# Kernel tuning notes

Hardware: AMD Instinct MI355X
Metric: run time of the kernel (lower is better)

Reference implementation:

```python
import jax, jax.numpy as jnp
import numpy as np

B, T, C = 2, 2048, 2048
H, D = 16, 128
ROPE_THETA = 100000.0


def _rms_norm(x):
    eps = jnp.asarray(jnp.finfo(x.dtype).eps, x.dtype)
    var = jnp.mean(jnp.square(x), axis=-1, keepdims=True)
    return x * jax.lax.rsqrt(var + eps)


def _apply_rotary(x, cos, sin):
    # x: [B,T,H,D]; cos/sin: [T,1,D//2] broadcasting over (B, H)
    d = x.shape[-1] // 2
    x1, x2 = x[..., :d], x[..., d:]
    y1 = x1 * cos + x2 * sin
    y2 = -x1 * sin + x2 * cos
    return jnp.concatenate([y1, y2], axis=-1)


def setup_inputs() -> dict:
    key = jax.random.key(0)
    ks = jax.random.split(key, 5)
    x = jax.random.normal(ks[0], (B, T, C), dtype=jnp.float32)
    # rotary table (caller-provided, already offset-applied)
    inv_freq = 1.0 / (ROPE_THETA ** (np.arange(0, D // 2, dtype=np.float32) / (D // 2)))
    t = np.arange(T, dtype=np.float32)
    freqs = np.outer(t, inv_freq)  # [T, D//2]
    cos = jnp.asarray(np.cos(freqs))[:, None, :]  # [T,1,D//2]
    sin = jnp.asarray(np.sin(freqs))[:, None, :]
    std = 0.02
    Wq = jax.random.normal(ks[1], (C, C), dtype=jnp.float32) * std
    Wk = jax.random.normal(ks[2], (C, C), dtype=jnp.float32) * std
    Wv = jax.random.normal(ks[3], (C, C), dtype=jnp.float32) * std
    Wo = jax.random.normal(ks[4], (C, C), dtype=jnp.float32) * std
    return {"x": x, "cos": cos, "sin": sin, "Wq": Wq, "Wk": Wk, "Wv": Wv, "Wo": Wo}


def reference(x, cos, sin, Wq, Wk, Wv, Wo):
    b, t, _ = x.shape
    # torch Linear: y = x @ W.T
    q = (x @ Wq.T).reshape(b, t, H, D)
    k = (x @ Wk.T).reshape(b, t, H, D)
    v = (x @ Wv.T).reshape(b, t, H, D)
    # qk RMSNorm (qk_norm=True)
    q = _rms_norm(q)
    k = _rms_norm(k)
    # rotary
    q = _apply_rotary(q, cos, sin)
    k = _apply_rotary(k, cos, sin)
    # causal SDPA, scale = 1/sqrt(D)
    scale = 1.0 / jnp.sqrt(jnp.asarray(D, x.dtype))
    scores = jnp.einsum('bthd,bshd->bhts', q, k) * scale  # [B,H,T,T]
    causal = jnp.tril(jnp.ones((t, t), dtype=bool))
    scores = jnp.where(causal[None, None], scores, jnp.asarray(-jnp.inf, x.dtype))
    attn = jax.nn.softmax(scores, axis=-1)
    o = jnp.einsum('bhts,bshd->bthd', attn, v).reshape(b, t, H * D)
    return o @ Wo.T
```

## Files before the change

kernel.cpp:

```cpp
#include <hip/hip_runtime.h>

using u16 = unsigned short;
typedef __attribute__((ext_vector_type(8))) short short8;
typedef __attribute__((ext_vector_type(4))) float f32x4;

#define DEV __device__ __forceinline__

DEV float bf2f(u16 u) { union { unsigned i; float f; } v; v.i = (unsigned)u << 16; return v.f; }
DEV u16 f2bf(float f) {
  union { float f; unsigned i; } v; v.f = f;
  return (u16)((v.i + 0x7fffu + ((v.i >> 16) & 1u)) >> 16);
}
DEV void async16(void* lds, const void* g) {
  __builtin_amdgcn_global_load_lds((const __attribute__((address_space(1))) void*)g,
                                   (__attribute__((address_space(3))) void*)lds, 16, 0, 0);
}

__global__ __launch_bounds__(256) void cvt_bf16(const float* __restrict__ in,
                                                u16* __restrict__ out, int n) {
  int i = (blockIdx.x * 256 + threadIdx.x) * 8;
  if (i >= n) return;
  const float4* p = (const float4*)(in + i);
  float4 a = p[0], b = p[1];
  short8 o;
  o[0] = (short)f2bf(a.x); o[1] = (short)f2bf(a.y);
  o[2] = (short)f2bf(a.z); o[3] = (short)f2bf(a.w);
  o[4] = (short)f2bf(b.x); o[5] = (short)f2bf(b.y);
  o[6] = (short)f2bf(b.z); o[7] = (short)f2bf(b.w);
  *(short8*)(out + i) = o;
}

template <bool BF16OUT>
DEV void gemm_body(const u16* __restrict__ A, const u16* __restrict__ Bw,
                   void* __restrict__ C, u16* As, u16* Bs) {
  constexpr int KD = 2048, N = 2048;
  const int tid = threadIdx.x, lane = tid & 63, w = tid >> 6;
  const int wm = (w >> 1) * 64, wn = (w & 1) * 64;
  const int lr = lane & 15, lk = lane >> 4;
  const size_t m0 = (size_t)blockIdx.y * 128, n0 = (size_t)blockIdx.x * 128;

  f32x4 acc[4][4];
#pragma unroll
  for (int i = 0; i < 4; ++i)
#pragma unroll
    for (int j = 0; j < 4; ++j) acc[i][j] = (f32x4){0.f, 0.f, 0.f, 0.f};

  const int bo0 = tid * 16;
  for (int kt = 0; kt < KD; kt += 32) {
#pragma unroll
    for (int i = 0; i < 2; ++i) {
      int bo = i * 4096 + bo0;
      int row = bo >> 6, cb = bo & 63;
      async16((char*)As + i * 4096 + w * 1024,
              (const char*)A + ((m0 + row) * KD + kt) * 2 + cb);
    }
#pragma unroll
    for (int i = 0; i < 2; ++i) {
      int bo = i * 4096 + bo0;
      int row = bo >> 6, cb = bo & 63;
      async16((char*)Bs + i * 4096 + w * 1024,
              (const char*)Bw + ((n0 + row) * KD + kt) * 2 + cb);
    }
    __syncthreads();
    short8 a[4], b[4];
#pragma unroll
    for (int mi = 0; mi < 4; ++mi)
      a[mi] = *(const short8*)(As + (wm + mi * 16 + lr) * 32 + lk * 8);
#pragma unroll
    for (int ni = 0; ni < 4; ++ni)
      b[ni] = *(const short8*)(Bs + (wn + ni * 16 + lr) * 32 + lk * 8);
#pragma unroll
    for (int mi = 0; mi < 4; ++mi)
#pragma unroll
      for (int ni = 0; ni < 4; ++ni)
        acc[mi][ni] =
            __builtin_amdgcn_mfma_f32_16x16x32_bf16(a[mi], b[ni], acc[mi][ni], 0, 0, 0);
    __syncthreads();
  }
#pragma unroll
  for (int mi = 0; mi < 4; ++mi)
#pragma unroll
    for (int ni = 0; ni < 4; ++ni)
#pragma unroll
      for (int r = 0; r < 4; ++r) {
        size_t row = m0 + wm + mi * 16 + lk * 4 + r;
        size_t col = n0 + wn + ni * 16 + lr;
        if constexpr (BF16OUT)
          ((u16*)C)[row * N + col] = f2bf(acc[mi][ni][r]);
        else
          ((float*)C)[row * N + col] = acc[mi][ni][r];
      }
}

__global__ __launch_bounds__(256) void gemm_qkv(
    const u16* __restrict__ X, const u16* __restrict__ Wq, const u16* __restrict__ Wk,
    const u16* __restrict__ Wv, u16* __restrict__ Qo, u16* __restrict__ Ko,
    u16* __restrict__ Vo) {
  __shared__ u16 As[128 * 32], Bs[128 * 32];
  const u16* W = blockIdx.z == 0 ? Wq : (blockIdx.z == 1 ? Wk : Wv);
  u16* C = blockIdx.z == 0 ? Qo : (blockIdx.z == 1 ? Ko : Vo);
  gemm_body<true>(X, W, C, As, Bs);
}

__global__ __launch_bounds__(256) void gemm_out(const u16* __restrict__ A,
                                                const u16* __restrict__ W,
                                                float* __restrict__ C) {
  __shared__ u16 As[128 * 32], Bs[128 * 32];
  gemm_body<false>(A, W, C, As, Bs);
}

__global__ __launch_bounds__(256) void rmsrope(u16* __restrict__ q, u16* __restrict__ k,
                                               const float* __restrict__ cosb,
                                               const float* __restrict__ sinb) {
  int gw = blockIdx.x * 4 + (threadIdx.x >> 6);
  int lane = threadIdx.x & 63;
  u16* base = q;
  float pre = 0.088388347648318447f * 1.4426950408889634f;
  if (gw >= 65536) { base = k; gw -= 65536; pre = 1.0f; }
  int bt = gw >> 4, h = gw & 15, t = bt & 2047;
  u16* p = base + (size_t)bt * 2048 + h * 128;
  float x1 = bf2f(p[lane]), x2 = bf2f(p[lane + 64]);
  float ss = x1 * x1 + x2 * x2;
#pragma unroll
  for (int m = 1; m < 64; m <<= 1) ss += __shfl_xor(ss, m, 64);
  float rn = rsqrtf(ss * (1.0f / 128.0f) + 1.1920929e-7f) * pre;
  float c = cosb[t * 64 + lane], s = sinb[t * 64 + lane];
  float y1 = (x1 * c + x2 * s) * rn;
  float y2 = (x2 * c - x1 * s) * rn;
  p[lane] = f2bf(y1);
  p[lane + 64] = f2bf(y2);
}

__global__ __launch_bounds__(256) void transpose_v(const u16* __restrict__ v,
                                                   u16* __restrict__ vt) {
  __shared__ u16 tile[64][72];
  int bh = blockIdx.z, b = bh >> 4, h = bh & 15;
  int t0 = blockIdx.x * 64, d0 = blockIdx.y * 64;
  int tid = threadIdx.x;
  int rr = tid >> 3, ch = tid & 7;
#pragma unroll
  for (int p = 0; p < 2; ++p) {
    int t = rr + p * 32;
    const u16* src = v + ((size_t)(b * 2048 + t0 + t) * 2048 + h * 128 + d0 + ch * 8);
    *(short8*)&tile[t][ch * 8] = *(const short8*)src;
  }
  __syncthreads();
#pragma unroll
  for (int p = 0; p < 2; ++p) {
    int d = rr + p * 32;
    int oc = ch * 8;
    short8 val;
#pragma unroll
    for (int j = 0; j < 8; ++j) val[j] = (short)tile[oc + j][d];
    *(short8*)(vt + ((size_t)(bh * 128 + d0 + d) * 2048 + t0 + oc)) = val;
  }
}

__global__ __launch_bounds__(256) void attn_fwd(const u16* __restrict__ Q,
                                                const u16* __restrict__ K,
                                                const u16* __restrict__ Vt,
                                                u16* __restrict__ O) {
  __shared__ u16 Ks[64 * 128];
  __shared__ u16 Vs[128 * 64];
  __shared__ u16 Ps[4][16 * 72];
  const int tid = threadIdx.x, lane = tid & 63, w = tid >> 6;
  const int lr = lane & 15, lk = lane >> 4;
  const int bh = blockIdx.y, b = bh >> 4, h = bh & 15;
  const int q0 = blockIdx.x * 64;
  const int qw = q0 + w * 16;

  short8 aq[4];
  const u16* qptr = Q + ((size_t)(b * 2048 + qw + lr)) * 2048 + h * 128;
#pragma unroll
  for (int kk = 0; kk < 4; ++kk) aq[kk] = *(const short8*)(qptr + kk * 32 + lk * 8);

  float mrow[4], lrow[4];
  f32x4 o[8];
#pragma unroll
  for (int r = 0; r < 4; ++r) { mrow[r] = -__builtin_inff(); lrow[r] = 0.f; }
#pragma unroll
  for (int nd = 0; nd < 8; ++nd) o[nd] = (f32x4){0.f, 0.f, 0.f, 0.f};

  const char* kbase = (const char*)(K + ((size_t)b * 2048) * 2048 + h * 128);
  const char* vbase = (const char*)(Vt + (size_t)bh * 128 * 2048);
  const int ntiles = blockIdx.x + 1;
  const int bo0 = tid * 16;

  for (int kt = 0; kt < ntiles; ++kt) {
    const int kv0 = kt * 64;
#pragma unroll
    for (int i = 0; i < 4; ++i) {
      int bo = i * 4096 + bo0;
      int r = bo >> 8, cb = bo & 255;
      async16((char*)Ks + i * 4096 + w * 1024,
              kbase + (size_t)(kv0 + r) * 4096 + (cb ^ ((r & 7) << 4)));
    }
#pragma unroll
    for (int i = 0; i < 4; ++i) {
      int bo = i * 4096 + bo0;
      int d = bo >> 7, cb = bo & 127;
      async16((char*)Vs + i * 4096 + w * 1024,
              vbase + (size_t)d * 4096 + (size_t)kv0 * 2 + (cb ^ ((d & 7) << 4)));
    }
    __syncthreads();

    f32x4 s[4];
#pragma unroll
    for (int n = 0; n < 4; ++n) {
      s[n] = (f32x4){0.f, 0.f, 0.f, 0.f};
#pragma unroll
      for (int kk = 0; kk < 4; ++kk) {
        int row = n * 16 + lr;
        int cb = kk * 64 + lk * 16;
        short8 bk = *(const short8*)((const char*)Ks + row * 256 + (cb ^ ((row & 7) << 4)));
        s[n] = __builtin_amdgcn_mfma_f32_16x16x32_bf16(aq[kk], bk, s[n], 0, 0, 0);
      }
    }
    if (kt == ntiles - 1) {
#pragma unroll
      for (int n = 0; n < 4; ++n)
#pragma unroll
        for (int r = 0; r < 4; ++r) {
          int col = kv0 + n * 16 + lr;
          int row = qw + lk * 4 + r;
          if (col > row) s[n][r] = -__builtin_inff();
        }
    }
    float al[4];
#pragma unroll
    for (int r = 0; r < 4; ++r) {
      float mx = fmaxf(fmaxf(s[0][r], s[1][r]), fmaxf(s[2][r], s[3][r]));
      mx = fmaxf(mx, __shfl_xor(mx, 1, 64));
      mx = fmaxf(mx, __shfl_xor(mx, 2, 64));
      mx = fmaxf(mx, __shfl_xor(mx, 4, 64));
      mx = fmaxf(mx, __shfl_xor(mx, 8, 64));
      float mn = fmaxf(mrow[r], mx);
      al[r] = exp2f(mrow[r] - mn);
      mrow[r] = mn;
    }
    float rs[4] = {0.f, 0.f, 0.f, 0.f};
#pragma unroll
    for (int n = 0; n < 4; ++n)
#pragma unroll
      for (int r = 0; r < 4; ++r) {
        float pv = exp2f(s[n][r] - mrow[r]);
        s[n][r] = pv;
        rs[r] += pv;
      }
#pragma unroll
    for (int r = 0; r < 4; ++r) {
      float t = rs[r];
      t += __shfl_xor(t, 1, 64); t += __shfl_xor(t, 2, 64);
      t += __shfl_xor(t, 4, 64); t += __shfl_xor(t, 8, 64);
      lrow[r] = lrow[r] * al[r] + t;
    }
#pragma unroll
    for (int nd = 0; nd < 8; ++nd)
#pragma unroll
      for (int r = 0; r < 4; ++r) o[nd][r] *= al[r];

    u16* pw = Ps[w];
#pragma unroll
    for (int n = 0; n < 4; ++n)
#pragma unroll
      for (int r = 0; r < 4; ++r)
        pw[(lk * 4 + r) * 72 + n * 16 + lr] = f2bf(s[n][r]);

#pragma unroll
    for (int kk = 0; kk < 2; ++kk) {
      short8 pa = *(const short8*)(pw + lr * 72 + kk * 32 + lk * 8);
#pragma unroll
      for (int nd = 0; nd < 8; ++nd) {
        int dr = nd * 16 + lr;
        int cb = kk * 64 + lk * 16;
        short8 bv = *(const short8*)((const char*)Vs + dr * 128 + (cb ^ ((dr & 7) << 4)));
        o[nd] = __builtin_amdgcn_mfma_f32_16x16x32_bf16(pa, bv, o[nd], 0, 0, 0);
      }
    }
    __syncthreads();
  }

  u16* op = O + ((size_t)(b * 2048 + qw + lk * 4)) * 2048 + h * 128;
#pragma unroll
  for (int r = 0; r < 4; ++r) {
    float inv = 1.0f / lrow[r];
#pragma unroll
    for (int nd = 0; nd < 8; ++nd)
      op[(size_t)r * 2048 + nd * 16 + lr] = f2bf(o[nd][r] * inv);
  }
}

extern "C" void kernel_launch(void* const* d_in, const int* in_sizes, int n_in,
                              void* d_out, int out_size, void* d_ws, size_t ws_size,
                              hipStream_t stream) {
  const float* x = (const float*)d_in[0];
  const float* cosb = (const float*)d_in[1];
  const float* sinb = (const float*)d_in[2];
  const float* Wq = (const float*)d_in[3];
  const float* Wk = (const float*)d_in[4];
  const float* Wv = (const float*)d_in[5];
  const float* Wo = (const float*)d_in[6];
  float* out = (float*)d_out;
  char* ws = (char*)d_ws;

  const size_t XB = (size_t)4096 * 2048 * 2;
  const size_t WB = (size_t)2048 * 2048 * 2;
  u16* xb  = (u16*)(ws);
  u16* wqb = (u16*)(ws + XB);
  u16* wkb = (u16*)(ws + XB + WB);
  u16* wvb = (u16*)(ws + XB + 2 * WB);
  u16* wob = (u16*)(ws + XB + 3 * WB);
  u16* qb  = (u16*)(ws + XB + 4 * WB);
  u16* kb  = (u16*)(ws + XB + 4 * WB + XB);
  u16* vb  = (u16*)(ws + XB + 4 * WB + 2 * XB);
  u16* vtb = (u16*)(ws + XB + 4 * WB + 3 * XB);
  u16* ob  = (u16*)(ws + XB + 4 * WB + 4 * XB);

  cvt_bf16<<<4096, 256, 0, stream>>>(x, xb, 8388608);
  cvt_bf16<<<2048, 256, 0, stream>>>(Wq, wqb, 4194304);
  cvt_bf16<<<2048, 256, 0, stream>>>(Wk, wkb, 4194304);
  cvt_bf16<<<2048, 256, 0, stream>>>(Wv, wvb, 4194304);
  cvt_bf16<<<2048, 256, 0, stream>>>(Wo, wob, 4194304);
  gemm_qkv<<<dim3(16, 32, 3), 256, 0, stream>>>(xb, wqb, wkb, wvb, qb, kb, vb);
  rmsrope<<<32768, 256, 0, stream>>>(qb, kb, cosb, sinb);
  transpose_v<<<dim3(32, 2, 32), 256, 0, stream>>>(vb, vtb);
  attn_fwd<<<dim3(32, 32), 256, 0, stream>>>(qb, kb, vtb, ob);
  gemm_out<<<dim3(16, 32), 256, 0, stream>>>(ob, wob, out);
}
```

Measured before the change: 524.1 us.

## Pair causal query tiles per block and widen attention KV tiles to 128

Each attention block now processes two 64-row query tiles, qt and 31-qt, so every block gets a similar amount of causal work, and the grid is halved to 16x32. The KV tile grows from 64 to 128 keys, which halves the barrier and load rounds per query tile. On the diagonal tile, fully masked 16-column sub-blocks skip their QK MFMAs. The P scratch buffer becomes XOR-swizzled instead of padded. In exchange, LDS use roughly doubles, which lowers occupancy, and each block runs its two tiles one after the other.

Measured after the change: 477.4 us. 8.9% less time.

```diff
diff --git a/kernel.cpp b/kernel.cpp
--- a/kernel.cpp
+++ b/kernel.cpp
@@ -160,133 +160,149 @@
                                                 const u16* __restrict__ K,
                                                 const u16* __restrict__ Vt,
                                                 u16* __restrict__ O) {
-  __shared__ u16 Ks[64 * 128];
-  __shared__ u16 Vs[128 * 64];
-  __shared__ u16 Ps[4][16 * 72];
+  __shared__ u16 Ks[128 * 128];
+  __shared__ u16 Vs[128 * 128];
+  __shared__ u16 Ps[4][16 * 128];
   const int tid = threadIdx.x, lane = tid & 63, w = tid >> 6;
   const int lr = lane & 15, lk = lane >> 4;
   const int bh = blockIdx.y, b = bh >> 4, h = bh & 15;
-  const int q0 = blockIdx.x * 64;
-  const int qw = q0 + w * 16;
-
-  short8 aq[4];
-  const u16* qptr = Q + ((size_t)(b * 2048 + qw + lr)) * 2048 + h * 128;
-#pragma unroll
-  for (int kk = 0; kk < 4; ++kk) aq[kk] = *(const short8*)(qptr + kk * 32 + lk * 8);
-
-  float mrow[4], lrow[4];
-  f32x4 o[8];
-#pragma unroll
-  for (int r = 0; r < 4; ++r) { mrow[r] = -__builtin_inff(); lrow[r] = 0.f; }
-#pragma unroll
-  for (int nd = 0; nd < 8; ++nd) o[nd] = (f32x4){0.f, 0.f, 0.f, 0.f};
 
   const char* kbase = (const char*)(K + ((size_t)b * 2048) * 2048 + h * 128);
   const char* vbase = (const char*)(Vt + (size_t)bh * 128 * 2048);
-  const int ntiles = blockIdx.x + 1;
   const int bo0 = tid * 16;
-
-  for (int kt = 0; kt < ntiles; ++kt) {
-    const int kv0 = kt * 64;
-#pragma unroll
-    for (int i = 0; i < 4; ++i) {
-      int bo = i * 4096 + bo0;
-      int r = bo >> 8, cb = bo & 255;
-      async16((char*)Ks + i * 4096 + w * 1024,
-              kbase + (size_t)(kv0 + r) * 4096 + (cb ^ ((r & 7) << 4)));
+  u16* pw = Ps[w];
+
+  for (int qi = 0; qi < 2; ++qi) {
+    const int qt = qi ? (31 - (int)blockIdx.x) : (int)blockIdx.x;
+    const int qw = qt * 64 + w * 16;
+    const int nt = (qt >> 1) + 1;
+    const int nlim = (qt & 1) ? 8 : 4;
+
+    short8 aq[4];
+    const u16* qptr = Q + ((size_t)(b * 2048 + qw + lr)) * 2048 + h * 128;
+#pragma unroll
+    for (int kk = 0; kk < 4; ++kk) aq[kk] = *(const short8*)(qptr + kk * 32 + lk * 8);
+
+    float mrow[4], lrow[4];
+    f32x4 o[8];
+#pragma unroll
+    for (int r = 0; r < 4; ++r) { mrow[r] = -__builtin_inff(); lrow[r] = 0.f; }
+#pragma unroll
+    for (int nd = 0; nd < 8; ++nd) o[nd] = (f32x4){0.f, 0.f, 0.f, 0.f};
+
+    for (int kt = 0; kt < nt; ++kt) {
+      const int kv0 = kt * 128;
+      const bool diag = (kt == nt - 1);
+#pragma unroll
+      for (int i = 0; i < 8; ++i) {
+        int bo = i * 4096 + bo0;
+        int r = bo >> 8, cb = bo & 255;
+        async16((char*)Ks + i * 4096 + w * 1024,
+                kbase + (size_t)(kv0 + r) * 4096 + (cb ^ ((r & 7) << 4)));
+      }
+#pragma unroll
+      for (int i = 0; i < 8; ++i) {
+        int bo = i * 4096 + bo0;
+        int d = bo >> 8, cb = bo & 255;
+        async16((char*)Vs + i * 4096 + w * 1024,
+                vbase + (size_t)d * 4096 + (size_t)kv0 * 2 + (cb ^ ((d & 7) << 4)));
+      }
+      __syncthreads();
+
+      f32x4 s[8];
+#pragma unroll
+      for (int n = 0; n < 8; ++n) {
+        s[n] = (f32x4){-__builtin_inff(), -__builtin_inff(), -__builtin_inff(),
+                       -__builtin_inff()};
+        if (!diag || n < nlim) {
+          f32x4 t = (f32x4){0.f, 0.f, 0.f, 0.f};
+#pragma unroll
+          for (int kk = 0; kk < 4; ++kk) {
+            int row = n * 16 + lr;
+            int cb = kk * 64 + lk * 16;
+            short8 bk =
+                *(const short8*)((const char*)Ks + row * 256 + (cb ^ ((row & 7) << 4)));
+            t = __builtin_amdgcn_mfma_f32_16x16x32_bf16(aq[kk], bk, t, 0, 0, 0);
+          }
+          s[n] = t;
+        }
+      }
+      if (diag) {
+#pragma unroll
+        for (int n = 0; n < 8; ++n)
+#pragma unroll
+          for (int r = 0; r < 4; ++r) {
+            int col = kv0 + n * 16 + lr;
+            int row = qw + lk * 4 + r;
+            if (col > row) s[n][r] = -__builtin_inff();
+          }
+      }
+      float al[4];
+#pragma unroll
+      for (int r = 0; r < 4; ++r) {
+        float mx = s[0][r];
+#pragma unroll
+        for (int n = 1; n < 8; ++n) mx = fmaxf(mx, s[n][r]);
+        mx = fmaxf(mx, __shfl_xor(mx, 1, 64));
+        mx = fmaxf(mx, __shfl_xor(mx, 2, 64));
+        mx = fmaxf(mx, __shfl_xor(mx, 4, 64));
+        mx = fmaxf(mx, __shfl_xor(mx, 8, 64));
+        float mn = fmaxf(mrow[r], mx);
+        al[r] = exp2f(mrow[r] - mn);
+        mrow[r] = mn;
+      }
+      float rs[4] = {0.f, 0.f, 0.f, 0.f};
+#pragma unroll
+      for (int n = 0; n < 8; ++n)
+#pragma unroll
+        for (int r = 0; r < 4; ++r) {
+          float pv = exp2f(s[n][r] - mrow[r]);
+          s[n][r] = pv;
+          rs[r] += pv;
+        }
+#pragma unroll
+      for (int r = 0; r < 4; ++r) {
+        float t = rs[r];
+        t += __shfl_xor(t, 1, 64); t += __shfl_xor(t, 2, 64);
+        t += __shfl_xor(t, 4, 64); t += __shfl_xor(t, 8, 64);
+        lrow[r] = lrow[r] * al[r] + t;
+      }
+#pragma unroll
+      for (int nd = 0; nd < 8; ++nd)
+#pragma unroll
+        for (int r = 0; r < 4; ++r) o[nd][r] *= al[r];
+
+#pragma unroll
+      for (int n = 0; n < 8; ++n)
+#pragma unroll
+        for (int r = 0; r < 4; ++r) {
+          int prow = lk * 4 + r;
+          pw[prow * 128 + ((n * 16 + lr) ^ ((prow & 7) << 3))] = f2bf(s[n][r]);
+        }
+
+#pragma unroll
+      for (int kk = 0; kk < 4; ++kk) {
+        short8 pa = *(const short8*)(pw + lr * 128 + ((kk * 32 + lk * 8) ^ ((lr & 7) << 3)));
+#pragma unroll
+        for (int nd = 0; nd < 8; ++nd) {
+          int dr = nd * 16 + lr;
+          int cb = kk * 64 + lk * 16;
+          short8 bv =
+              *(const short8*)((const char*)Vs + dr * 256 + (cb ^ ((dr & 7) << 4)));
+          o[nd] = __builtin_amdgcn_mfma_f32_16x16x32_bf16(pa, bv, o[nd], 0, 0, 0);
+        }
+      }
+      __syncthreads();
     }
-#pragma unroll
-    for (int i = 0; i < 4; ++i) {
-      int bo = i * 4096 + bo0;
-      int d = bo >> 7, cb = bo & 127;
-      async16((char*)Vs + i * 4096 + w * 1024,
-              vbase + (size_t)d * 4096 + (size_t)kv0 * 2 + (cb ^ ((d & 7) << 4)));
+
+    u16* op = O + ((size_t)(b * 2048 + qw + lk * 4)) * 2048 + h * 128;
+#pragma unroll
+    for (int r = 0; r < 4; ++r) {
+      float inv = 1.0f / lrow[r];
+#pragma unroll
+      for (int nd = 0; nd < 8; ++nd)
+        op[(size_t)r * 2048 + nd * 16 + lr] = f2bf(o[nd][r] * inv);
     }
-    __syncthreads();
-
-    f32x4 s[4];
-#pragma unroll
-    for (int n = 0; n < 4; ++n) {
-      s[n] = (f32x4){0.f, 0.f, 0.f, 0.f};
-#pragma unroll
-      for (int kk = 0; kk < 4; ++kk) {
-        int row = n * 16 + lr;
-        int cb = kk * 64 + lk * 16;
-        short8 bk = *(const short8*)((const char*)Ks + row * 256 + (cb ^ ((row & 7) << 4)));
-        s[n] = __builtin_amdgcn_mfma_f32_16x16x32_bf16(aq[kk], bk, s[n], 0, 0, 0);
-      }
-    }
-    if (kt == ntiles - 1) {
-#pragma unroll
-      for (int n = 0; n < 4; ++n)
-#pragma unroll
-        for (int r = 0; r < 4; ++r) {
-          int col = kv0 + n * 16 + lr;
-          int row = qw + lk * 4 + r;
-          if (col > row) s[n][r] = -__builtin_inff();
-        }
-    }
-    float al[4];
-#pragma unroll
-    for (int r = 0; r < 4; ++r) {
-      float mx = fmaxf(fmaxf(s[0][r], s[1][r]), fmaxf(s[2][r], s[3][r]));
-      mx = fmaxf(mx, __shfl_xor(mx, 1, 64));
-      mx = fmaxf(mx, __shfl_xor(mx, 2, 64));
-      mx = fmaxf(mx, __shfl_xor(mx, 4, 64));
-      mx = fmaxf(mx, __shfl_xor(mx, 8, 64));
-      float mn = fmaxf(mrow[r], mx);
-      al[r] = exp2f(mrow[r] - mn);
-      mrow[r] = mn;
-    }
-    float rs[4] = {0.f, 0.f, 0.f, 0.f};
-#pragma unroll
-    for (int n = 0; n < 4; ++n)
-#pragma unroll
-      for (int r = 0; r < 4; ++r) {
-        float pv = exp2f(s[n][r] - mrow[r]);
-        s[n][r] = pv;
-        rs[r] += pv;
-      }
-#pragma unroll
-    for (int r = 0; r < 4; ++r) {
-      float t = rs[r];
-      t += __shfl_xor(t, 1, 64); t += __shfl_xor(t, 2, 64);
-      t += __shfl_xor(t, 4, 64); t += __shfl_xor(t, 8, 64);
-      lrow[r] = lrow[r] * al[r] + t;
-    }
-#pragma unroll
-    for (int nd = 0; nd < 8; ++nd)
-#pragma unroll
-      for (int r = 0; r < 4; ++r) o[nd][r] *= al[r];
-
-    u16* pw = Ps[w];
-#pragma unroll
-    for (int n = 0; n < 4; ++n)
-#pragma unroll
-      for (int r = 0; r < 4; ++r)
-        pw[(lk * 4 + r) * 72 + n * 16 + lr] = f2bf(s[n][r]);
-
-#pragma unroll
-    for (int kk = 0; kk < 2; ++kk) {
-      short8 pa = *(const short8*)(pw + lr * 72 + kk * 32 + lk * 8);
-#pragma unroll
-      for (int nd = 0; nd < 8; ++nd) {
-        int dr = nd * 16 + lr;
-        int cb = kk * 64 + lk * 16;
-        short8 bv = *(const short8*)((const char*)Vs + dr * 128 + (cb ^ ((dr & 7) << 4)));
-        o[nd] = __builtin_amdgcn_mfma_f32_16x16x32_bf16(pa, bv, o[nd], 0, 0, 0);
-      }
-    }
-    __syncthreads();
-  }
-
-  u16* op = O + ((size_t)(b * 2048 + qw + lk * 4)) * 2048 + h * 128;
-#pragma unroll
-  for (int r = 0; r < 4; ++r) {
-    float inv = 1.0f / lrow[r];
-#pragma unroll
-    for (int nd = 0; nd < 8; ++nd)
-      op[(size_t)r * 2048 + nd * 16 + lr] = f2bf(o[nd][r] * inv);
   }
 }
 
@@ -324,6 +340,6 @@
   gemm_qkv<<<dim3(16, 32, 3), 256, 0, stream>>>(xb, wqb, wkb, wvb, qb, kb, vb);
   rmsrope<<<32768, 256, 0, stream>>>(qb, kb, cosb, sinb);
   transpose_v<<<dim3(32, 2, 32), 256, 0, stream>>>(vb, vtb);
-  attn_fwd<<<dim3(32, 32), 256, 0, stream>>>(qb, kb, vtb, ob);
+  attn_fwd<<<dim3(16, 32), 256, 0, stream>>>(qb, kb, vtb, ob);
   gemm_out<<<dim3(16, 32), 256, 0, stream>>>(ob, wob, out);
 }
```
